# Kernel optimization log

Hardware: AMD Instinct MI355X
Metric: run time of the kernel (lower is better)

## Reference

```python
import jax, jax.numpy as jnp
import numpy as np

EPS_BN = 1e-5  # torch BatchNorm1d default eps


def setup_inputs() -> dict:
    key = jax.random.key(0)
    k1, k2, k3 = jax.random.split(key, 3)
    B, C, L = 512, 8, 16384
    attn_maps = jax.random.normal(k1, (B, C, L), dtype=jnp.float32)
    target_matrix = jax.random.uniform(k2, (B, C, C), dtype=jnp.float32)
    conv_bias = jnp.ones((C,), dtype=jnp.float32) * 0.5  # nn.Parameter(torch.ones(8)/2)
    w_fc = jax.random.normal(k3, (3, 1), dtype=jnp.float32) * 0.1
    b_fc = jnp.zeros((3,), dtype=jnp.float32)
    return {"attn_maps": attn_maps, "target_matrix": target_matrix,
            "conv_bias": conv_bias, "w_fc": w_fc, "b_fc": b_fc}


def reference(attn_maps, target_matrix, conv_bias, w_fc, b_fc):
    B, C, L = attn_maps.shape  # C == 8 (fixed by the grouped 1x1 conv)
    # (attn - mean of per-row means) * 100; rows are uniform length so this is the global mean
    x = (attn_maps - jnp.mean(attn_maps)) * 100.0
    # grouped conv1d, kernel 1, weight == 5: per-channel affine, then sigmoid / 5
    bin_maps = jax.nn.sigmoid(5.0 * x + conv_bias[None, :, None]) / 5.0  # (B, C, L)
    b5 = bin_maps * 5.0
    # vectorized triangular IoU: intersection / union over the length dim
    inter = jnp.einsum('bil,bjl->bij', b5, b5)                     # (B, C, C)
    union = L - jnp.einsum('bil,bjl->bij', 1.0 - b5, 1.0 - b5)      # (B, C, C)
    tril = jnp.tril(jnp.ones((C, C), dtype=bool))
    sim = jnp.where(tril, inter / union, 0.0)
    # rep_type 'abs': sum of |sim - 100*target| over the lower triangle (incl. diag)
    tm = target_matrix * 100.0
    st = jnp.sum(jnp.where(tril, jnp.abs(sim - tm), 0.0), axis=(1, 2))  # (B,)
    # BatchNorm1d(1, affine=False) in training mode: normalize over the batch
    mu = jnp.mean(st)
    var = jnp.var(st)  # biased variance, as torch BN uses for normalization
    st_n = (st - mu) * jax.lax.rsqrt(var + EPS_BN)                  # (B,)
    # final linear 1 -> 3 (original Linear(128,3) is shape-inconsistent; see notes)
    out = st_n[:, None] @ w_fc.T + b_fc                              # (B, 3)
    return out
```

## Files before the change

kernel.cpp:

```cpp
#include <hip/hip_runtime.h>
#include <math.h>

typedef float f32x4 __attribute__((ext_vector_type(4)));

#define B_DIM 512
#define C_DIM 8
#define L_DIM 16384
#define NELEM (B_DIM * C_DIM * L_DIM)
#define LOG2E 1.4426950408889634f
#define KA (-500.0f * LOG2E)

#if __has_builtin(__builtin_amdgcn_exp2f)
#define EXP2F __builtin_amdgcn_exp2f
#else
#define EXP2F exp2f
#endif

#define H_NODE 0.25
#define F_P 1.2840254166877414f
#define F_M 0.7788007830714049f

#define TRI(i, j) ((i) * ((i) + 1) / 2 + (j))

#define WS_GRAM_OFF 8192

__global__ __launch_bounds__(256) void k_main(const f32x4* __restrict__ in4,
                                              const float* __restrict__ bias,
                                              float* __restrict__ asum,
                                              float* __restrict__ gram_t) {
  const int tid = threadIdx.x;
  const int lane = tid & 63, wv = tid >> 6;
  const int nodesel = tid >> 7;
  const int pt = tid & 127;
  const int b = blockIdx.x >> 1, half = blockIdx.x & 1;

  const float Fn = nodesel ? F_M : F_P;
  float kc[8];
#pragma unroll
  for (int c = 0; c < 8; ++c) kc[c] = bias[c] * (-LOG2E);

  float acc[44];
#pragma unroll
  for (int k = 0; k < 44; ++k) acc[k] = 0.f;
  float asacc = 0.f;

  const f32x4* base = in4 + (size_t)b * (8 * 4096) + half * 2048 + pt;

#pragma unroll 1
  for (int it = 0; it < 16; ++it) {
    f32x4 v[8];
#pragma unroll
    for (int c = 0; c < 8; ++c) v[c] = base[c * 4096 + it * 128];
#pragma unroll
    for (int e = 0; e < 4; ++e) {
      float s[8];
#pragma unroll
      for (int c = 0; c < 8; ++c) {
        float a = (e == 0) ? v[c].x : (e == 1) ? v[c].y : (e == 2) ? v[c].z : v[c].w;
        if (nodesel == 0) asacc += a;
        float E = EXP2F(fmaf(KA, a, kc[c]));
        s[c] = __builtin_amdgcn_rcpf(fmaf(E, Fn, 1.f));
        acc[c] += s[c];
      }
#pragma unroll
      for (int i = 0; i < 8; ++i)
#pragma unroll
        for (int j = 0; j <= i; ++j)
          acc[8 + TRI(i, j)] = fmaf(s[i], s[j], acc[8 + TRI(i, j)]);
    }
  }

  __shared__ float lgr[4][44];
  __shared__ float las[2];
#pragma unroll
  for (int k = 0; k < 44; ++k) {
    float x = acc[k];
#pragma unroll
    for (int off = 32; off; off >>= 1) x += __shfl_xor(x, off, 64);
    if (lane == 0) lgr[wv][k] = x;
  }
  if (nodesel == 0) {
    float x = asacc;
#pragma unroll
    for (int off = 32; off; off >>= 1) x += __shfl_xor(x, off, 64);
    if (lane == 0) las[wv] = x;
  }
  __syncthreads();
  if (tid < 88) {
    const int n = tid / 44, k = tid - n * 44;
    const float r = lgr[2 * n][k] + lgr[2 * n + 1][k];
    gram_t[(size_t)(half * 88 + n * 44 + k) * 512 + b] = r;
  }
  if (tid == 96) asum[blockIdx.x] = las[0] + las[1];
}

__global__ __launch_bounds__(512) void k_final(const float* __restrict__ asum,
                                               const float* __restrict__ gram_t,
                                               const float* __restrict__ target,
                                               const float* __restrict__ w_fc,
                                               const float* __restrict__ b_fc,
                                               float* __restrict__ out) {
  const int t = threadIdx.x;
  __shared__ double red[512];

  red[t] = (double)asum[t] + (double)asum[t + 512];
  __syncthreads();
  for (int off = 256; off; off >>= 1) {
    if (t < off) red[t] += red[t + off];
    __syncthreads();
  }
  const double th = 500.0 * (red[0] / (double)NELEM);
  __syncthreads();

  const double w0 = (th + H_NODE) / (2.0 * H_NODE);
  const double w1 = (H_NODE - th) / (2.0 * H_NODE);

  double S[8], T[36];
#pragma unroll
  for (int i = 0; i < 8; ++i) S[i] = 0.0;
#pragma unroll
  for (int k = 0; k < 36; ++k) T[k] = 0.0;
#pragma unroll
  for (int h = 0; h < 2; ++h) {
    const float* g = gram_t + (size_t)h * 88 * 512 + t;
#pragma unroll
    for (int i = 0; i < 8; ++i)
      S[i] += w0 * (double)g[(0 + i) * 512] + w1 * (double)g[(44 + i) * 512];
#pragma unroll
    for (int k = 0; k < 36; ++k)
      T[k] += w0 * (double)g[(8 + k) * 512] + w1 * (double)g[(52 + k) * 512];
  }

  double st = 0.0;
#pragma unroll
  for (int i = 0; i < 8; ++i)
#pragma unroll
    for (int j = 0; j <= i; ++j) {
      double inter = T[TRI(i, j)];
      double uni = (S[i] + S[j]) - inter;
      double sim = inter / uni;
      double tm = 100.0 * (double)target[t * 64 + i * 8 + j];
      st += fabs(sim - tm);
    }

  red[t] = st;
  __syncthreads();
  for (int off = 256; off; off >>= 1) {
    if (t < off) red[t] += red[t + off];
    __syncthreads();
  }
  const double mean = red[0] * (1.0 / 512.0);
  __syncthreads();
  const double dd = st - mean;
  red[t] = dd * dd;
  __syncthreads();
  for (int off = 256; off; off >>= 1) {
    if (t < off) red[t] += red[t + off];
    __syncthreads();
  }
  const double var = red[0] * (1.0 / 512.0);
  const float stn = (float)((st - mean) / sqrt(var + 1e-5));
#pragma unroll
  for (int k = 0; k < 3; ++k)
    out[t * 3 + k] = fmaf(stn, w_fc[k], b_fc[k]);
}

extern "C" void kernel_launch(void* const* d_in, const int* in_sizes, int n_in,
                              void* d_out, int out_size, void* d_ws, size_t ws_size,
                              hipStream_t stream) {
  const float* attn   = (const float*)d_in[0];
  const float* target = (const float*)d_in[1];
  const float* bias   = (const float*)d_in[2];
  const float* w_fc   = (const float*)d_in[3];
  const float* b_fc   = (const float*)d_in[4];
  float* out = (float*)d_out;
  float* ws  = (float*)d_ws;

  float* asum   = ws;
  float* gram_t = ws + WS_GRAM_OFF;

  k_main<<<1024, 256, 0, stream>>>((const f32x4*)attn, bias, asum, gram_t);
  k_final<<<1, 512, 0, stream>>>(asum, gram_t, target, w_fc, b_fc, out);
}
```

Before: 86.95 us.

## Accumulate sigmoid Gram products with packed fp16 dot2 and one block per batch

Sigmoid values for pairs of elements are packed into fp16x2 and accumulated with v_dot2_f32_f16, which halves the FMA count for the 36 Gram entries and the 8 row sums. The grid is also cut from 1024 to 512 blocks, each covering a full batch row, so the final kernel no longer merges two halves. The cost is fp16 rounding of the sigmoid values, which could hurt the IoU accuracy, and fewer blocks for latency hiding on a memory-bound stream.

```diff
diff --git a/kernel.cpp b/kernel.cpp
--- a/kernel.cpp
+++ b/kernel.cpp
@@ -2,6 +2,7 @@
 #include <math.h>
 
 typedef float f32x4 __attribute__((ext_vector_type(4)));
+typedef _Float16 f16x2 __attribute__((ext_vector_type(2)));
 
 #define B_DIM 512
 #define C_DIM 8
@@ -14,6 +15,12 @@
 #define EXP2F __builtin_amdgcn_exp2f
 #else
 #define EXP2F exp2f
+#endif
+
+#if __has_builtin(__builtin_amdgcn_fdot2)
+#define HAVE_FDOT2 1
+#else
+#define HAVE_FDOT2 0
 #endif
 
 #define H_NODE 0.25
@@ -32,41 +39,63 @@
   const int lane = tid & 63, wv = tid >> 6;
   const int nodesel = tid >> 7;
   const int pt = tid & 127;
-  const int b = blockIdx.x >> 1, half = blockIdx.x & 1;
+  const int b = blockIdx.x;
 
   const float Fn = nodesel ? F_M : F_P;
-  float kc[8];
-#pragma unroll
-  for (int c = 0; c < 8; ++c) kc[c] = bias[c] * (-LOG2E);
+  float kc[C_DIM];
+#pragma unroll
+  for (int c = 0; c < C_DIM; ++c) kc[c] = bias[c] * (-LOG2E);
 
   float acc[44];
 #pragma unroll
   for (int k = 0; k < 44; ++k) acc[k] = 0.f;
   float asacc = 0.f;
 
-  const f32x4* base = in4 + (size_t)b * (8 * 4096) + half * 2048 + pt;
+#if HAVE_FDOT2
+  const f16x2 ONE2 = {(_Float16)1.f, (_Float16)1.f};
+#endif
+
+  const f32x4* base = in4 + (size_t)b * (C_DIM * 4096) + pt;
 
 #pragma unroll 1
-  for (int it = 0; it < 16; ++it) {
-    f32x4 v[8];
-#pragma unroll
-    for (int c = 0; c < 8; ++c) v[c] = base[c * 4096 + it * 128];
-#pragma unroll
-    for (int e = 0; e < 4; ++e) {
-      float s[8];
-#pragma unroll
-      for (int c = 0; c < 8; ++c) {
-        float a = (e == 0) ? v[c].x : (e == 1) ? v[c].y : (e == 2) ? v[c].z : v[c].w;
-        if (nodesel == 0) asacc += a;
-        float E = EXP2F(fmaf(KA, a, kc[c]));
-        s[c] = __builtin_amdgcn_rcpf(fmaf(E, Fn, 1.f));
-        acc[c] += s[c];
+  for (int it = 0; it < 32; ++it) {
+    f32x4 v[C_DIM];
+#pragma unroll
+    for (int c = 0; c < C_DIM; ++c) v[c] = base[c * 4096 + it * 128];
+#pragma unroll
+    for (int p = 0; p < 2; ++p) {
+      float sx[C_DIM], sy[C_DIM];
+#if HAVE_FDOT2
+      f16x2 s2[C_DIM];
+#endif
+#pragma unroll
+      for (int c = 0; c < C_DIM; ++c) {
+        const float ax = p ? v[c].z : v[c].x;
+        const float ay = p ? v[c].w : v[c].y;
+        if (nodesel == 0) asacc += ax + ay;
+        const float Ex = EXP2F(fmaf(KA, ax, kc[c]));
+        const float Ey = EXP2F(fmaf(KA, ay, kc[c]));
+        sx[c] = __builtin_amdgcn_rcpf(fmaf(Ex, Fn, 1.f));
+        sy[c] = __builtin_amdgcn_rcpf(fmaf(Ey, Fn, 1.f));
+#if HAVE_FDOT2
+        s2[c] = __builtin_bit_cast(f16x2, __builtin_amdgcn_cvt_pkrtz(sx[c], sy[c]));
+        acc[c] = __builtin_amdgcn_fdot2(s2[c], ONE2, acc[c], false);
+#else
+        acc[c] += sx[c] + sy[c];
+#endif
       }
 #pragma unroll
-      for (int i = 0; i < 8; ++i)
-#pragma unroll
-        for (int j = 0; j <= i; ++j)
-          acc[8 + TRI(i, j)] = fmaf(s[i], s[j], acc[8 + TRI(i, j)]);
+      for (int i = 0; i < C_DIM; ++i)
+#pragma unroll
+        for (int j = 0; j <= i; ++j) {
+#if HAVE_FDOT2
+          acc[8 + TRI(i, j)] =
+              __builtin_amdgcn_fdot2(s2[i], s2[j], acc[8 + TRI(i, j)], false);
+#else
+          acc[8 + TRI(i, j)] =
+              fmaf(sx[i], sx[j], fmaf(sy[i], sy[j], acc[8 + TRI(i, j)]));
+#endif
+        }
     }
   }
 
@@ -88,10 +117,9 @@
   __syncthreads();
   if (tid < 88) {
     const int n = tid / 44, k = tid - n * 44;
-    const float r = lgr[2 * n][k] + lgr[2 * n + 1][k];
-    gram_t[(size_t)(half * 88 + n * 44 + k) * 512 + b] = r;
-  }
-  if (tid == 96) asum[blockIdx.x] = las[0] + las[1];
+    gram_t[(size_t)(n * 44 + k) * 512 + b] = lgr[2 * n][k] + lgr[2 * n + 1][k];
+  }
+  if (tid == 96) asum[b] = las[0] + las[1];
 }
 
 __global__ __launch_bounds__(512) void k_final(const float* __restrict__ asum,
@@ -103,7 +131,7 @@
   const int t = threadIdx.x;
   __shared__ double red[512];
 
-  red[t] = (double)asum[t] + (double)asum[t + 512];
+  red[t] = (double)asum[t];
   __syncthreads();
   for (int off = 256; off; off >>= 1) {
     if (t < off) red[t] += red[t + off];
@@ -115,21 +143,14 @@
   const double w0 = (th + H_NODE) / (2.0 * H_NODE);
   const double w1 = (H_NODE - th) / (2.0 * H_NODE);
 
+  const float* g = gram_t + t;
   double S[8], T[36];
 #pragma unroll
-  for (int i = 0; i < 8; ++i) S[i] = 0.0;
-#pragma unroll
-  for (int k = 0; k < 36; ++k) T[k] = 0.0;
-#pragma unroll
-  for (int h = 0; h < 2; ++h) {
-    const float* g = gram_t + (size_t)h * 88 * 512 + t;
-#pragma unroll
-    for (int i = 0; i < 8; ++i)
-      S[i] += w0 * (double)g[(0 + i) * 512] + w1 * (double)g[(44 + i) * 512];
-#pragma unroll
-    for (int k = 0; k < 36; ++k)
-      T[k] += w0 * (double)g[(8 + k) * 512] + w1 * (double)g[(52 + k) * 512];
-  }
+  for (int i = 0; i < 8; ++i)
+    S[i] = w0 * (double)g[(0 + i) * 512] + w1 * (double)g[(44 + i) * 512];
+#pragma unroll
+  for (int k = 0; k < 36; ++k)
+    T[k] = w0 * (double)g[(8 + k) * 512] + w1 * (double)g[(52 + k) * 512];
 
   double st = 0.0;
 #pragma unroll
@@ -179,6 +200,6 @@
   float* asum   = ws;
   float* gram_t = ws + WS_GRAM_OFF;
 
-  k_main<<<1024, 256, 0, stream>>>((const f32x4*)attn, bias, asum, gram_t);
+  k_main<<<B_DIM, 256, 0, stream>>>((const f32x4*)attn, bias, asum, gram_t);
   k_final<<<1, 512, 0, stream>>>(asum, gram_t, target, w_fc, b_fc, out);
 }
```

New measurement: 86.75 us. No clear change (-0.2%).

## Compute Gram sums with fp16 MFMA over LDS-staged double-buffered tiles

Applied to the files above, without the earlier changes.

The per-batch 8x8 Gram accumulation moves off scalar FMAs onto MFMA 16x16x32 f16 instructions. Each block handles a pair of batches, so 16 channel rows form one 16x16 product. Input tiles are streamed into swizzled LDS through global_load_lds with double buffering, and the final kernel is updated for the new workspace layout. This removes about 36 FMAs per element and the large accumulator register footprint, at the cost of rounding the sigmoid values to fp16 and adding barrier and LDS staging overhead.

```diff
diff --git a/kernel.cpp b/kernel.cpp
--- a/kernel.cpp
+++ b/kernel.cpp
@@ -2,6 +2,8 @@
 #include <math.h>
 
 typedef float f32x4 __attribute__((ext_vector_type(4)));
+typedef __fp16 h16x2 __attribute__((ext_vector_type(2)));
+typedef _Float16 f16x8 __attribute__((ext_vector_type(8)));
 
 #define B_DIM 512
 #define C_DIM 8
@@ -22,76 +24,131 @@
 
 #define TRI(i, j) ((i) * ((i) + 1) / 2 + (j))
 
+#define NT 16
+#define TILE_B 32768
+
 #define WS_GRAM_OFF 8192
 
-__global__ __launch_bounds__(256) void k_main(const f32x4* __restrict__ in4,
+typedef const __attribute__((address_space(1))) unsigned int gu32_t;
+typedef __attribute__((address_space(3))) unsigned int lu32_t;
+__device__ __forceinline__ void gload_lds16(const void* g, void* l) {
+  __builtin_amdgcn_global_load_lds((gu32_t*)g, (lu32_t*)l, 16, 0, 0);
+}
+
+__global__ __launch_bounds__(256) void k_main(const float* __restrict__ in,
                                               const float* __restrict__ bias,
                                               float* __restrict__ asum,
                                               float* __restrict__ gram_t) {
   const int tid = threadIdx.x;
   const int lane = tid & 63, wv = tid >> 6;
-  const int nodesel = tid >> 7;
-  const int pt = tid & 127;
-  const int b = blockIdx.x >> 1, half = blockIdx.x & 1;
-
-  const float Fn = nodesel ? F_M : F_P;
-  float kc[8];
-#pragma unroll
-  for (int c = 0; c < 8; ++c) kc[c] = bias[c] * (-LOG2E);
-
-  float acc[44];
-#pragma unroll
-  for (int k = 0; k < 44; ++k) acc[k] = 0.f;
-  float asacc = 0.f;
-
-  const f32x4* base = in4 + (size_t)b * (8 * 4096) + half * 2048 + pt;
+  const int node = wv >> 1, sub = wv & 1;
+  const int ch = lane & 15, kgrp = lane >> 4;
+  const int p = blockIdx.x >> 1, half = blockIdx.x & 1;
+
+  __shared__ char smem[2 * TILE_B];
+
+  const float Fn = node ? F_M : F_P;
+  const float kc = bias[ch & 7] * (-LOG2E);
+
+  f32x4 acc = {0.f, 0.f, 0.f, 0.f};
+  float ssum = 0.f, asacc = 0.f;
+
+  const float* gback = in + (size_t)p * 16 * L_DIM + half * 8192;
+
+  auto stage = [&](int t, int d) {
+#pragma unroll
+    for (int ci = 0; ci < 4; ++ci) {
+      const int c = wv * 4 + ci;
+      const float* grow = gback + (size_t)c * L_DIM + t * 512;
+#pragma unroll
+      for (int q = 0; q < 2; ++q) {
+        const int srcb = (q * 1024 + lane * 16) ^ (c << 4);
+        char* l = smem + d * TILE_B + c * 2048 + q * 1024;
+        gload_lds16((const void*)(grow + (srcb >> 2)), (void*)l);
+      }
+    }
+  };
+
+  auto consume = [&](int d) {
+#pragma unroll
+    for (int j = 0; j < 8; ++j) {
+      const int k = sub * 8 + j;
+      const int o = k * 128 + kgrp * 32;
+      const char* lb = smem + d * TILE_B + ch * 2048;
+      const int A1 = o ^ (ch << 4);
+      f32x4 v1 = *(const f32x4*)(lb + A1);
+      f32x4 v2 = *(const f32x4*)(lb + (A1 ^ 16));
+      float s[8];
+#pragma unroll
+      for (int e = 0; e < 8; ++e) {
+        const float a = (e < 4) ? ((e == 0) ? v1.x : (e == 1) ? v1.y : (e == 2) ? v1.z : v1.w)
+                                : ((e == 4) ? v2.x : (e == 5) ? v2.y : (e == 6) ? v2.z : v2.w);
+        if (node == 0) asacc += a;
+        const float E = EXP2F(fmaf(KA, a, kc));
+        s[e] = __builtin_amdgcn_rcpf(fmaf(E, Fn, 1.f));
+        ssum += s[e];
+      }
+      union { f16x8 v; h16x2 h[4]; } u;
+      u.h[0] = __builtin_amdgcn_cvt_pkrtz(s[0], s[1]);
+      u.h[1] = __builtin_amdgcn_cvt_pkrtz(s[2], s[3]);
+      u.h[2] = __builtin_amdgcn_cvt_pkrtz(s[4], s[5]);
+      u.h[3] = __builtin_amdgcn_cvt_pkrtz(s[6], s[7]);
+      acc = __builtin_amdgcn_mfma_f32_16x16x32_f16(u.v, u.v, acc, 0, 0, 0);
+    }
+  };
+
+  stage(0, 0);
+  stage(1, 1);
 
 #pragma unroll 1
-  for (int it = 0; it < 16; ++it) {
-    f32x4 v[8];
-#pragma unroll
-    for (int c = 0; c < 8; ++c) v[c] = base[c * 4096 + it * 128];
-#pragma unroll
-    for (int e = 0; e < 4; ++e) {
-      float s[8];
-#pragma unroll
-      for (int c = 0; c < 8; ++c) {
-        float a = (e == 0) ? v[c].x : (e == 1) ? v[c].y : (e == 2) ? v[c].z : v[c].w;
-        if (nodesel == 0) asacc += a;
-        float E = EXP2F(fmaf(KA, a, kc[c]));
-        s[c] = __builtin_amdgcn_rcpf(fmaf(E, Fn, 1.f));
-        acc[c] += s[c];
-      }
-#pragma unroll
-      for (int i = 0; i < 8; ++i)
-#pragma unroll
-        for (int j = 0; j <= i; ++j)
-          acc[8 + TRI(i, j)] = fmaf(s[i], s[j], acc[8 + TRI(i, j)]);
-    }
-  }
-
-  __shared__ float lgr[4][44];
-  __shared__ float las[2];
-#pragma unroll
-  for (int k = 0; k < 44; ++k) {
-    float x = acc[k];
-#pragma unroll
-    for (int off = 32; off; off >>= 1) x += __shfl_xor(x, off, 64);
-    if (lane == 0) lgr[wv][k] = x;
-  }
-  if (nodesel == 0) {
+  for (int t = 0; t < NT; ++t) {
+    const int d = t & 1;
+    if (t < NT - 1) {
+      asm volatile("s_waitcnt vmcnt(8)" ::: "memory");
+    } else {
+      asm volatile("s_waitcnt vmcnt(0)" ::: "memory");
+    }
+    __builtin_amdgcn_s_barrier();
+    consume(d);
+    __builtin_amdgcn_s_barrier();
+    if (t + 2 < NT) stage(t + 2, d);
+  }
+  __syncthreads();
+
+  ssum += __shfl_xor(ssum, 16, 64);
+  ssum += __shfl_xor(ssum, 32, 64);
+
+  float* lgr = (float*)smem;
+  float* lss = (float*)(smem + 4096);
+  float* las = (float*)(smem + 4096 + 256);
+#pragma unroll
+  for (int r = 0; r < 4; ++r) lgr[wv * 256 + lane * 4 + r] = acc[r];
+  if (lane < 16) lss[wv * 16 + lane] = ssum;
+  if (node == 0) {
     float x = asacc;
 #pragma unroll
     for (int off = 32; off; off >>= 1) x += __shfl_xor(x, off, 64);
     if (lane == 0) las[wv] = x;
   }
   __syncthreads();
-  if (tid < 88) {
-    const int n = tid / 44, k = tid - n * 44;
-    const float r = lgr[2 * n][k] + lgr[2 * n + 1][k];
-    gram_t[(size_t)(half * 88 + n * 44 + k) * 512 + b] = r;
-  }
-  if (tid == 96) asum[blockIdx.x] = las[0] + las[1];
+
+#pragma unroll
+  for (int n = 0; n < 2; ++n) {
+    if (tid < 272) {
+      float val;
+      if (tid < 256) {
+        const int row = tid >> 4, col = tid & 15;
+        const int lsrc = col | ((row >> 2) << 4), reg = row & 3;
+        val = lgr[(n * 2 + 0) * 256 + lsrc * 4 + reg] +
+              lgr[(n * 2 + 1) * 256 + lsrc * 4 + reg];
+      } else {
+        const int c = tid - 256;
+        val = lss[(n * 2 + 0) * 16 + c] + lss[(n * 2 + 1) * 16 + c];
+      }
+      gram_t[((size_t)((half * 2 + n) * 272) + tid) * 256 + p] = val;
+    }
+  }
+  if (tid == 0) asum[blockIdx.x] = las[0] + las[1];
 }
 
 __global__ __launch_bounds__(512) void k_final(const float* __restrict__ asum,
@@ -101,9 +158,10 @@
                                                const float* __restrict__ b_fc,
                                                float* __restrict__ out) {
   const int t = threadIdx.x;
+  const int pair = t >> 1, r0 = (t & 1) * 8;
   __shared__ double red[512];
 
-  red[t] = (double)asum[t] + (double)asum[t + 512];
+  red[t] = (double)asum[t];
   __syncthreads();
   for (int off = 256; off; off >>= 1) {
     if (t < off) red[t] += red[t + off];
@@ -122,13 +180,19 @@
   for (int k = 0; k < 36; ++k) T[k] = 0.0;
 #pragma unroll
   for (int h = 0; h < 2; ++h) {
-    const float* g = gram_t + (size_t)h * 88 * 512 + t;
+    const float* g0 = gram_t + (size_t)((h * 2 + 0) * 272) * 256 + pair;
+    const float* g1 = gram_t + (size_t)((h * 2 + 1) * 272) * 256 + pair;
 #pragma unroll
     for (int i = 0; i < 8; ++i)
-      S[i] += w0 * (double)g[(0 + i) * 512] + w1 * (double)g[(44 + i) * 512];
-#pragma unroll
-    for (int k = 0; k < 36; ++k)
-      T[k] += w0 * (double)g[(8 + k) * 512] + w1 * (double)g[(52 + k) * 512];
+      S[i] += w0 * (double)g0[(256 + r0 + i) * 256] +
+              w1 * (double)g1[(256 + r0 + i) * 256];
+#pragma unroll
+    for (int i = 0; i < 8; ++i)
+#pragma unroll
+      for (int j = 0; j <= i; ++j) {
+        const int e = (r0 + i) * 16 + (r0 + j);
+        T[TRI(i, j)] += w0 * (double)g0[e * 256] + w1 * (double)g1[e * 256];
+      }
   }
 
   double st = 0.0;
@@ -179,6 +243,6 @@
   float* asum   = ws;
   float* gram_t = ws + WS_GRAM_OFF;
 
-  k_main<<<1024, 256, 0, stream>>>((const f32x4*)attn, bias, asum, gram_t);
+  k_main<<<B_DIM, 256, 0, stream>>>(attn, bias, asum, gram_t);
   k_final<<<1, 512, 0, stream>>>(asum, gram_t, target, w_fc, b_fc, out);
 }
```

Result: faster. 81.78 us (-5.9%).
